# Performance work log

Hardware: AMD Instinct MI355X
Metric: run time of the kernel (lower is better)

Reference implementation:

```python
import jax, jax.numpy as jnp
import numpy as np

N, K, F, H = 10000, 32, 128, 256  # nodes, max_neighbors, edge_feat_dim, hidden_size
EPS = 1e-5


def layer_norm(x, g, b):
    m = jnp.mean(x, axis=-1, keepdims=True)
    v = jnp.mean(jnp.square(x - m), axis=-1, keepdims=True)
    return (x - m) * jax.lax.rsqrt(v + EPS) * g + b


def setup_inputs() -> dict:
    key = jax.random.key(0)
    ks = jax.random.split(key, 8)
    edge_features = jax.random.normal(ks[0], (N, K, F), dtype=jnp.float32)
    neighbor_mask = jax.random.randint(ks[1], (N, K), 0, 2) > 0
    s_lin = 1.0 / np.sqrt(F)
    s_h = 1.0 / np.sqrt(H)
    return {
        "edge_features": edge_features,
        "neighbor_mask": neighbor_mask,
        "W_lin": jax.random.normal(ks[2], (F, H), dtype=jnp.float32) * s_lin,
        "b_lin": jnp.zeros((H,), dtype=jnp.float32),
        "g_pre": jnp.ones((H,), dtype=jnp.float32),
        "b_pre": jnp.zeros((H,), dtype=jnp.float32),
        "W_ff1": jax.random.normal(ks[3], (H, H), dtype=jnp.float32) * s_h,
        "b_ff1": jnp.zeros((H,), dtype=jnp.float32),
        "W_ff2": jax.random.normal(ks[4], (H, H), dtype=jnp.float32) * s_h,
        "b_ff2": jnp.zeros((H,), dtype=jnp.float32),
        "g_node": jnp.ones((H,), dtype=jnp.float32),
        "b_node": jnp.zeros((H,), dtype=jnp.float32),
        "g_edge": jnp.ones((H,), dtype=jnp.float32),
        "b_edge": jnp.zeros((H,), dtype=jnp.float32),
    }


def reference(edge_features, neighbor_mask, W_lin, b_lin, g_pre, b_pre,
              W_ff1, b_ff1, W_ff2, b_ff2, g_node, b_node, g_edge, b_edge):
    # edge linear: [N,K,F] @ [F,H] -> [N,K,H]
    edge_hidden = jnp.einsum("nkf,fh->nkh", edge_features, W_lin) + b_lin
    # pre-norm FFN with residual
    h = layer_norm(edge_hidden, g_pre, b_pre)
    h = jax.nn.gelu(jnp.einsum("nkh,hd->nkd", h, W_ff1) + b_ff1)
    h = jnp.einsum("nkd,dh->nkh", h, W_ff2) + b_ff2
    edge_output = edge_hidden + h
    # masked neighbor aggregation (segment-style reduce over padded neighbors)
    node_output = jnp.sum(
        jnp.where(neighbor_mask[:, :, None], edge_output, 0.0), axis=1)
    # output normalization on both node and edge features
    node_out = layer_norm(node_output, g_node, b_node)
    edge_out = layer_norm(edge_output, g_edge, b_edge)
    return (node_out, edge_out)
```

## Files before the change

kernel.cpp:

```cpp
#include <hip/hip_runtime.h>

typedef float f32x4 __attribute__((ext_vector_type(4)));
typedef float f32x2 __attribute__((ext_vector_type(2)));
typedef short bf16x8 __attribute__((ext_vector_type(8)));
typedef unsigned int u32;
typedef unsigned int u32x2 __attribute__((ext_vector_type(2)));
typedef unsigned short u16;

#define DEVI static __device__ __forceinline__

static constexpr int HD    = 256;
static constexpr int NNODE = 10000;

DEVI u16 f2bf(float f) {
  u32 u = __builtin_bit_cast(u32, f);
  u = (u + 0x7fffu + ((u >> 16) & 1u)) >> 16;
  return (u16)u;
}
DEVI float bf2f(u16 s) {
  u32 u = ((u32)s) << 16;
  return __builtin_bit_cast(float, u);
}
DEVI float gelu_f(float y) {
  float z = 0.7978845608028654f * (y + 0.044715f * y * y * y);
  float E = __expf(2.f * z);
  return y * (1.f - 1.f / (E + 1.f));
}

__global__ void prep_weights(const float* __restrict__ W_lin, const float* __restrict__ g_pre,
                             const float* __restrict__ W_ff1, const float* __restrict__ W_ff2,
                             u16* __restrict__ Wlt, u16* __restrict__ W1gt, u16* __restrict__ W2t)
{
  int e = blockIdx.x * 256 + threadIdx.x;
  if (e < 32768) {
    int c = e >> 7, k = e & 127;
    Wlt[e] = f2bf(W_lin[k * 256 + c]);
  } else if (e < 32768 + 65536) {
    int e2 = e - 32768; int c = e2 >> 8, k = e2 & 255;
    W1gt[e2] = f2bf(g_pre[k] * W_ff1[k * 256 + c]);
  } else if (e < 163840) {
    int e3 = e - 98304; int c = e3 >> 8, k = e3 & 255;
    W2t[e3] = f2bf(W_ff2[k * 256 + c]);
  }
}

__global__ void prep_uv(const float* __restrict__ W_ff1, const float* __restrict__ g_pre,
                        const float* __restrict__ b_pre, const float* __restrict__ b_ff1,
                        float* __restrict__ u, float* __restrict__ v)
{
  int c = threadIdx.x;
  float uu = 0.f, vv = 0.f;
#pragma unroll 8
  for (int k = 0; k < 256; ++k) {
    float w = W_ff1[k * 256 + c];
    uu += g_pre[k] * w;
    vv += b_pre[k] * w;
  }
  u[c] = uu;
  v[c] = vv + b_ff1[c];
}

template<int NK, int STRIDE>
DEVI void run_gemm(f32x4 (&acc)[4][4], const char* __restrict__ xbase,
                   const u16* __restrict__ Wt, int lo, int hi, int wc)
{
  const char* __restrict__ wp = (const char*)Wt;
#pragma unroll
  for (int ks = 0; ks < NK; ++ks) {
    bf16x8 a[4], b[4];
#pragma unroll
    for (int nt = 0; nt < 4; ++nt) {
      int cc = wc * 64 + nt * 16 + lo;
      b[nt] = *(const bf16x8*)(wp + (size_t)cc * (NK * 64) + ks * 64 + hi * 16);
    }
#pragma unroll
    for (int rg = 0; rg < 4; ++rg) {
      int r = rg * 16 + lo;
      a[rg] = *(const bf16x8*)(xbase + r * STRIDE + (((ks * 4 + hi) ^ (r & 7)) << 4));
    }
#pragma unroll
    for (int nt = 0; nt < 4; ++nt)
#pragma unroll
      for (int rg = 0; rg < 4; ++rg)
        acc[rg][nt] = __builtin_amdgcn_mfma_f32_16x16x32_bf16(b[nt], a[rg], acc[rg][nt], 0, 0, 0);
  }
}

__global__ __launch_bounds__(256, 3)
void mega_kernel(const float* __restrict__ EF, const int* __restrict__ nmask,
                 const u16* __restrict__ Wlt, const u16* __restrict__ W1gt, const u16* __restrict__ W2t,
                 const float* __restrict__ b_lin, const float* __restrict__ uc, const float* __restrict__ vc,
                 const float* __restrict__ b_ff2, const float* __restrict__ g_edge, const float* __restrict__ b_edge,
                 const float* __restrict__ g_node, const float* __restrict__ b_node,
                 float* __restrict__ node_out, float* __restrict__ edge_out)
{
  const int tid  = threadIdx.x;
  const int lane = tid & 63;
  const int wc   = tid >> 6;
  const int lo   = lane & 15;
  const int hi   = lane >> 4;
  const int tile0 = blockIdx.x * 64;

  __shared__ char  xLDS[32768];
  __shared__ float part[4][64][2];
  __shared__ int   lm[64];
  __shared__ float red[4][2];

  if (tid < 64) lm[tid] = nmask[tile0 + tid];

#pragma unroll
  for (int it = 0; it < 4; ++it) {
    int idx = it * 256 + tid;
    int r = idx >> 4, sl = idx & 15;
    const float* src = EF + (size_t)(tile0 + r) * 128 + sl * 8;
    f32x4 x0 = __builtin_nontemporal_load((const f32x4*)src);
    f32x4 x1 = __builtin_nontemporal_load((const f32x4*)(src + 4));
    bf16x8 t;
    t[0] = (short)f2bf(x0[0]); t[1] = (short)f2bf(x0[1]);
    t[2] = (short)f2bf(x0[2]); t[3] = (short)f2bf(x0[3]);
    t[4] = (short)f2bf(x1[0]); t[5] = (short)f2bf(x1[1]);
    t[6] = (short)f2bf(x1[2]); t[7] = (short)f2bf(x1[3]);
    *(bf16x8*)(xLDS + r * 256 + ((sl ^ (r & 7)) << 4)) = t;
  }
  __syncthreads();

  f32x4 acc[4][4];
#pragma unroll
  for (int rg = 0; rg < 4; ++rg)
#pragma unroll
    for (int nt = 0; nt < 4; ++nt) acc[rg][nt] = f32x4{0.f, 0.f, 0.f, 0.f};

  run_gemm<4, 256>(acc, xLDS, Wlt, lo, hi, wc);

  u32x2 ehreg[4][4];
  {
    f32x4 bl[4];
#pragma unroll
    for (int nt = 0; nt < 4; ++nt)
      bl[nt] = *(const f32x4*)(b_lin + wc * 64 + nt * 16 + hi * 4);
#pragma unroll
    for (int rg = 0; rg < 4; ++rg) {
      int r = rg * 16 + lo;
      float ss = 0.f, qq = 0.f;
#pragma unroll
      for (int nt = 0; nt < 4; ++nt) {
        f32x4 x = acc[rg][nt] + bl[nt];
        u32 w0 = (u32)f2bf(x[0]) | ((u32)f2bf(x[1]) << 16);
        u32 w1 = (u32)f2bf(x[2]) | ((u32)f2bf(x[3]) << 16);
        ehreg[rg][nt] = u32x2{w0, w1};
        ss += x[0] + x[1] + x[2] + x[3];
        qq += x[0]*x[0] + x[1]*x[1] + x[2]*x[2] + x[3]*x[3];
      }
      ss += __shfl_xor(ss, 16); ss += __shfl_xor(ss, 32);
      qq += __shfl_xor(qq, 16); qq += __shfl_xor(qq, 32);
      if (hi == 0) { part[wc][r][0] = ss; part[wc][r][1] = qq; }
    }
  }
  __syncthreads();
  if (tid < 64) {
    float ss = part[0][tid][0] + part[1][tid][0] + part[2][tid][0] + part[3][tid][0];
    float qq = part[0][tid][1] + part[1][tid][1] + part[2][tid][1] + part[3][tid][1];
    float m  = ss * (1.f / 256.f);
    float var = qq * (1.f / 256.f) - m * m;
    part[0][tid][0] = m;
    part[0][tid][1] = rsqrtf(var + 1e-5f);
  }
#pragma unroll
  for (int rg = 0; rg < 4; ++rg) {
    int r = rg * 16 + lo;
#pragma unroll
    for (int nt = 0; nt < 4; ++nt) {
      int slot = wc * 8 + nt * 2 + (hi >> 1);
      *(u32x2*)(xLDS + r * 512 + ((slot ^ (r & 7)) << 4) + (hi & 1) * 8) = ehreg[rg][nt];
    }
  }
  __syncthreads();

#pragma unroll
  for (int rg = 0; rg < 4; ++rg)
#pragma unroll
    for (int nt = 0; nt < 4; ++nt) acc[rg][nt] = f32x4{0.f, 0.f, 0.f, 0.f};
  run_gemm<8, 512>(acc, xLDS, W1gt, lo, hi, wc);
  __syncthreads();

  {
    f32x4 u4[4], v4[4];
#pragma unroll
    for (int nt = 0; nt < 4; ++nt) {
      u4[nt] = *(const f32x4*)(uc + wc * 64 + nt * 16 + hi * 4);
      v4[nt] = *(const f32x4*)(vc + wc * 64 + nt * 16 + hi * 4);
    }
#pragma unroll
    for (int rg = 0; rg < 4; ++rg) {
      int r = rg * 16 + lo;
      float m  = part[0][r][0];
      float rs = part[0][r][1];
      float rm = m * rs;
#pragma unroll
      for (int nt = 0; nt < 4; ++nt) {
        f32x4 y = acc[rg][nt] * rs - u4[nt] * rm + v4[nt];
        u32 w0 = (u32)f2bf(gelu_f(y[0])) | ((u32)f2bf(gelu_f(y[1])) << 16);
        u32 w1 = (u32)f2bf(gelu_f(y[2])) | ((u32)f2bf(gelu_f(y[3])) << 16);
        int slot = wc * 8 + nt * 2 + (hi >> 1);
        *(u32x2*)(xLDS + r * 512 + ((slot ^ (r & 7)) << 4) + (hi & 1) * 8) = u32x2{w0, w1};
      }
    }
  }
  __syncthreads();

#pragma unroll
  for (int rg = 0; rg < 4; ++rg)
#pragma unroll
    for (int nt = 0; nt < 4; ++nt) acc[rg][nt] = f32x4{0.f, 0.f, 0.f, 0.f};
  run_gemm<8, 512>(acc, xLDS, W2t, lo, hi, wc);

  {
    f32x4 b2[4];
#pragma unroll
    for (int nt = 0; nt < 4; ++nt)
      b2[nt] = *(const f32x4*)(b_ff2 + wc * 64 + nt * 16 + hi * 4);
#pragma unroll
    for (int rg = 0; rg < 4; ++rg) {
      int r = rg * 16 + lo;
      float ss = 0.f, qq = 0.f;
#pragma unroll
      for (int nt = 0; nt < 4; ++nt) {
        f32x4 x = acc[rg][nt] + b2[nt];
        x[0] += bf2f((u16)(ehreg[rg][nt][0] & 0xffffu));
        x[1] += bf2f((u16)(ehreg[rg][nt][0] >> 16));
        x[2] += bf2f((u16)(ehreg[rg][nt][1] & 0xffffu));
        x[3] += bf2f((u16)(ehreg[rg][nt][1] >> 16));
        acc[rg][nt] = x;
        ss += x[0] + x[1] + x[2] + x[3];
        qq += x[0]*x[0] + x[1]*x[1] + x[2]*x[2] + x[3]*x[3];
      }
      ss += __shfl_xor(ss, 16); ss += __shfl_xor(ss, 32);
      qq += __shfl_xor(qq, 16); qq += __shfl_xor(qq, 32);
      if (hi == 0) { part[wc][r][0] = ss; part[wc][r][1] = qq; }
    }
  }
  __syncthreads();
  if (tid < 64) {
    float ss = part[0][tid][0] + part[1][tid][0] + part[2][tid][0] + part[3][tid][0];
    float qq = part[0][tid][1] + part[1][tid][1] + part[2][tid][1] + part[3][tid][1];
    float m  = ss * (1.f / 256.f);
    float var = qq * (1.f / 256.f) - m * m;
    part[0][tid][0] = m;
    part[0][tid][1] = rsqrtf(var + 1e-5f);
  }
  __syncthreads();

  {
    f32x4 ge4[4], be4[4];
#pragma unroll
    for (int nt = 0; nt < 4; ++nt) {
      ge4[nt] = *(const f32x4*)(g_edge + wc * 64 + nt * 16 + hi * 4);
      be4[nt] = *(const f32x4*)(b_edge + wc * 64 + nt * 16 + hi * 4);
    }
#pragma unroll
    for (int rg = 0; rg < 4; ++rg) {
      int r = rg * 16 + lo;
      float m2  = part[0][r][0];
      float rs2 = part[0][r][1];
#pragma unroll
      for (int nt = 0; nt < 4; ++nt) {
        f32x4 x = acc[rg][nt];
        u32 w0 = (u32)f2bf(x[0]) | ((u32)f2bf(x[1]) << 16);
        u32 w1 = (u32)f2bf(x[2]) | ((u32)f2bf(x[3]) << 16);
        int slot = wc * 8 + nt * 2 + (hi >> 1);
        *(u32x2*)(xLDS + r * 512 + ((slot ^ (r & 7)) << 4) + (hi & 1) * 8) = u32x2{w0, w1};
        f32x4 o = (x - m2) * rs2 * ge4[nt] + be4[nt];
        __builtin_nontemporal_store(o,
            (f32x4*)(edge_out + (size_t)(tile0 + r) * 256 + wc * 64 + nt * 16 + hi * 4));
      }
    }
  }
  __syncthreads();

  {
    int nd = tid >> 7;
    int c0 = (tid & 127) * 2;
    int chunk = c0 >> 3;
    int wib = (c0 & 7) * 2;
    float s0 = 0.f, s1 = 0.f;
#pragma unroll
    for (int r32 = 0; r32 < 32; ++r32) {
      int r = nd * 32 + r32;
      if (lm[r] != 0) {
        u32 w = *(const u32*)(xLDS + r * 512 + ((chunk ^ (r & 7)) << 4) + wib);
        s0 += bf2f((u16)(w & 0xffffu));
        s1 += bf2f((u16)(w >> 16));
      }
    }
    float ss = s0 + s1, qq = s0 * s0 + s1 * s1;
#pragma unroll
    for (int d = 1; d < 64; d <<= 1) { ss += __shfl_xor(ss, d); qq += __shfl_xor(qq, d); }
    if (lane == 0) { red[wc][0] = ss; red[wc][1] = qq; }
    __syncthreads();
    ss = red[nd * 2][0] + red[nd * 2 + 1][0];
    qq = red[nd * 2][1] + red[nd * 2 + 1][1];
    float m   = ss * (1.f / 256.f);
    float var = qq * (1.f / 256.f) - m * m;
    float rs  = rsqrtf(var + 1e-5f);
    f32x2 gn = *(const f32x2*)(g_node + c0);
    f32x2 bn = *(const f32x2*)(b_node + c0);
    f32x2 o;
    o[0] = (s0 - m) * rs * gn[0] + bn[0];
    o[1] = (s1 - m) * rs * gn[1] + bn[1];
    __builtin_nontemporal_store(o,
        (f32x2*)(node_out + (size_t)(blockIdx.x * 2 + nd) * 256 + c0));
  }
}

extern "C" void kernel_launch(void* const* d_in, const int* in_sizes, int n_in,
                              void* d_out, int out_size, void* d_ws, size_t ws_size,
                              hipStream_t stream)
{
  (void)in_sizes; (void)n_in; (void)out_size; (void)ws_size;
  const float* edge_features = (const float*)d_in[0];
  const int*   nmask  = (const int*)d_in[1];
  const float* W_lin  = (const float*)d_in[2];
  const float* b_lin  = (const float*)d_in[3];
  const float* g_pre  = (const float*)d_in[4];
  const float* b_pre  = (const float*)d_in[5];
  const float* W_ff1  = (const float*)d_in[6];
  const float* b_ff1  = (const float*)d_in[7];
  const float* W_ff2  = (const float*)d_in[8];
  const float* b_ff2  = (const float*)d_in[9];
  const float* g_node = (const float*)d_in[10];
  const float* b_node = (const float*)d_in[11];
  const float* g_edge = (const float*)d_in[12];
  const float* b_edge = (const float*)d_in[13];

  char* ws = (char*)d_ws;
  u16* Wlt   = (u16*)ws;   ws += 256 * 128 * 2;
  u16* W1gt  = (u16*)ws;   ws += 256 * 256 * 2;
  u16* W2t   = (u16*)ws;   ws += 256 * 256 * 2;
  float* ucp = (float*)ws; ws += 256 * 4;
  float* vcp = (float*)ws; ws += 256 * 4;

  float* node_out = (float*)d_out;
  float* edge_out = (float*)d_out + (size_t)NNODE * HD;

  prep_weights<<<640, 256, 0, stream>>>(W_lin, g_pre, W_ff1, W_ff2, Wlt, W1gt, W2t);
  prep_uv<<<1, 256, 0, stream>>>(W_ff1, g_pre, b_pre, b_ff1, ucp, vcp);
  mega_kernel<<<5000, 256, 0, stream>>>(edge_features, nmask, Wlt, W1gt, W2t,
                                        b_lin, ucp, vcp, b_ff2, g_edge, b_edge,
                                        g_node, b_node, node_out, edge_out);
}
```

Before: 754.9 us.

## Use HIP bf16 conversion intrinsic, raise occupancy bound, drop nontemporal accesses

```diff
diff --git a/kernel.cpp b/kernel.cpp
--- a/kernel.cpp
+++ b/kernel.cpp
@@ -1,4 +1,5 @@
 #include <hip/hip_runtime.h>
+#include <hip/hip_bf16.h>
 
 typedef float f32x4 __attribute__((ext_vector_type(4)));
 typedef float f32x2 __attribute__((ext_vector_type(2)));
@@ -13,9 +14,11 @@
 static constexpr int NNODE = 10000;
 
 DEVI u16 f2bf(float f) {
-  u32 u = __builtin_bit_cast(u32, f);
-  u = (u + 0x7fffu + ((u >> 16) & 1u)) >> 16;
-  return (u16)u;
+  __hip_bfloat16 h = __float2bfloat16(f);
+  return __builtin_bit_cast(u16, h);
+}
+DEVI u32 f2bf2(float a, float b) {
+  return (u32)f2bf(a) | ((u32)f2bf(b) << 16);
 }
 DEVI float bf2f(u16 s) {
   u32 u = ((u32)s) << 16;
@@ -86,7 +89,7 @@
   }
 }
 
-__global__ __launch_bounds__(256, 3)
+__global__ __launch_bounds__(256, 4)
 void mega_kernel(const float* __restrict__ EF, const int* __restrict__ nmask,
                  const u16* __restrict__ Wlt, const u16* __restrict__ W1gt, const u16* __restrict__ W2t,
                  const float* __restrict__ b_lin, const float* __restrict__ uc, const float* __restrict__ vc,
@@ -113,13 +116,17 @@
     int idx = it * 256 + tid;
     int r = idx >> 4, sl = idx & 15;
     const float* src = EF + (size_t)(tile0 + r) * 128 + sl * 8;
-    f32x4 x0 = __builtin_nontemporal_load((const f32x4*)src);
-    f32x4 x1 = __builtin_nontemporal_load((const f32x4*)(src + 4));
+    f32x4 x0 = *(const f32x4*)src;
+    f32x4 x1 = *(const f32x4*)(src + 4);
     bf16x8 t;
-    t[0] = (short)f2bf(x0[0]); t[1] = (short)f2bf(x0[1]);
-    t[2] = (short)f2bf(x0[2]); t[3] = (short)f2bf(x0[3]);
-    t[4] = (short)f2bf(x1[0]); t[5] = (short)f2bf(x1[1]);
-    t[6] = (short)f2bf(x1[2]); t[7] = (short)f2bf(x1[3]);
+    u32 p0 = f2bf2(x0[0], x0[1]);
+    u32 p1 = f2bf2(x0[2], x0[3]);
+    u32 p2 = f2bf2(x1[0], x1[1]);
+    u32 p3 = f2bf2(x1[2], x1[3]);
+    t[0] = (short)(p0 & 0xffffu); t[1] = (short)(p0 >> 16);
+    t[2] = (short)(p1 & 0xffffu); t[3] = (short)(p1 >> 16);
+    t[4] = (short)(p2 & 0xffffu); t[5] = (short)(p2 >> 16);
+    t[6] = (short)(p3 & 0xffffu); t[7] = (short)(p3 >> 16);
     *(bf16x8*)(xLDS + r * 256 + ((sl ^ (r & 7)) << 4)) = t;
   }
   __syncthreads();
@@ -145,9 +152,7 @@
 #pragma unroll
       for (int nt = 0; nt < 4; ++nt) {
         f32x4 x = acc[rg][nt] + bl[nt];
-        u32 w0 = (u32)f2bf(x[0]) | ((u32)f2bf(x[1]) << 16);
-        u32 w1 = (u32)f2bf(x[2]) | ((u32)f2bf(x[3]) << 16);
-        ehreg[rg][nt] = u32x2{w0, w1};
+        ehreg[rg][nt] = u32x2{f2bf2(x[0], x[1]), f2bf2(x[2], x[3])};
         ss += x[0] + x[1] + x[2] + x[3];
         qq += x[0]*x[0] + x[1]*x[1] + x[2]*x[2] + x[3]*x[3];
       }
@@ -199,8 +204,8 @@
 #pragma unroll
       for (int nt = 0; nt < 4; ++nt) {
         f32x4 y = acc[rg][nt] * rs - u4[nt] * rm + v4[nt];
-        u32 w0 = (u32)f2bf(gelu_f(y[0])) | ((u32)f2bf(gelu_f(y[1])) << 16);
-        u32 w1 = (u32)f2bf(gelu_f(y[2])) | ((u32)f2bf(gelu_f(y[3])) << 16);
+        u32 w0 = f2bf2(gelu_f(y[0]), gelu_f(y[1]));
+        u32 w1 = f2bf2(gelu_f(y[2]), gelu_f(y[3]));
         int slot = wc * 8 + nt * 2 + (hi >> 1);
         *(u32x2*)(xLDS + r * 512 + ((slot ^ (r & 7)) << 4) + (hi & 1) * 8) = u32x2{w0, w1};
       }
@@ -265,13 +270,12 @@
 #pragma unroll
       for (int nt = 0; nt < 4; ++nt) {
         f32x4 x = acc[rg][nt];
-        u32 w0 = (u32)f2bf(x[0]) | ((u32)f2bf(x[1]) << 16);
-        u32 w1 = (u32)f2bf(x[2]) | ((u32)f2bf(x[3]) << 16);
+        u32 w0 = f2bf2(x[0], x[1]);
+        u32 w1 = f2bf2(x[2], x[3]);
         int slot = wc * 8 + nt * 2 + (hi >> 1);
         *(u32x2*)(xLDS + r * 512 + ((slot ^ (r & 7)) << 4) + (hi & 1) * 8) = u32x2{w0, w1};
         f32x4 o = (x - m2) * rs2 * ge4[nt] + be4[nt];
-        __builtin_nontemporal_store(o,
-            (f32x4*)(edge_out + (size_t)(tile0 + r) * 256 + wc * 64 + nt * 16 + hi * 4));
+        *(f32x4*)(edge_out + (size_t)(tile0 + r) * 256 + wc * 64 + nt * 16 + hi * 4) = o;
       }
     }
   }
@@ -307,8 +311,7 @@
     f32x2 o;
     o[0] = (s0 - m) * rs * gn[0] + bn[0];
     o[1] = (s1 - m) * rs * gn[1] + bn[1];
-    __builtin_nontemporal_store(o,
-        (f32x2*)(node_out + (size_t)(blockIdx.x * 2 + nd) * 256 + c0));
+    *(f32x2*)(node_out + (size_t)(blockIdx.x * 2 + nd) * 256 + c0) = o;
   }
 }
 
```

After: 759.6 us. About the same (+0.6%).
